# Kernel tuning notes

Measured on AMD Instinct MI355X. Metric: run time of the kernel, lower is better.

Reference implementation:

```python
import jax, jax.numpy as jnp
import numpy as np

T, N, D = 512, 1024, 256


def setup_inputs() -> dict:
    key = jax.random.key(0)
    k1, k2, k3, k4 = jax.random.split(key, 4)
    scale = 1.0 / np.sqrt(D)
    return {
        "H": jax.random.normal(k1, (T, N, D), dtype=jnp.float32),
        "fc_w": jax.random.normal(k2, (D, D), dtype=jnp.float32) * scale,
        "fc_b": jax.random.normal(k3, (D,), dtype=jnp.float32) * scale,
        "score_w": jax.random.normal(k4, (D,), dtype=jnp.float32) * scale,
    }


def _causal_attend(H, e):
    """C[t] = sum_{s<=t} softmax_{s<=t}(e[s]) * H[s], via online softmax scan.

    H: (T, N, D), e: (T, N) -> C: (T, N, D). O(T*N*D) time/memory.
    """
    n = H.shape[1]
    m0 = jnp.full((n,), -jnp.inf, dtype=H.dtype)   # running max of e
    s0 = jnp.zeros((n,), dtype=H.dtype)            # running softmax denom
    num0 = jnp.zeros((n, H.shape[2]), dtype=H.dtype)  # running weighted sum

    def step(carry, inp):
        m, s, num = carry
        e_t, h_t = inp  # (N,), (N, D)
        m_new = jnp.maximum(m, e_t)
        alpha = jnp.exp(m - m_new)          # rescale old accumulators
        p = jnp.exp(e_t - m_new)            # weight of current timestep
        s_new = s * alpha + p
        num_new = num * alpha[:, None] + p[:, None] * h_t
        c_t = num_new / s_new[:, None]
        return (m_new, s_new, num_new), c_t

    _, C = jax.lax.scan(step, (m0, s0, num0), (e, H))
    return C  # (T, N, D)


def reference(H, fc_w, fc_b, score_w):
    # Q = tanh(Linear(H)); e = score(Q)  -> (T, N)
    Q = jnp.tanh(jnp.einsum('tnd,ed->tne', H, fc_w) + fc_b)
    e = jnp.einsum('tne,e->tn', Q, score_w)
    return _causal_attend(H, e)
```

## Files before the change

kernel.cpp:

```cpp
#include <hip/hip_runtime.h>
#include <hip/hip_bf16.h>
#include <math.h>


#define T_DIM 512
#define N_DIM 1024
#define D_DIM 256

typedef short v8s __attribute__((ext_vector_type(8)));
typedef float v4f __attribute__((ext_vector_type(4)));

__device__ __forceinline__ unsigned pk_bf16(float a, float b) {
    unsigned ua = __builtin_bit_cast(unsigned, a);
    unsigned ub = __builtin_bit_cast(unsigned, b);
    ua = ua + 0x7fffu + ((ua >> 16) & 1u);
    ub = ub + 0x7fffu + ((ub >> 16) & 1u);
    return (ua >> 16) | (ub & 0xffff0000u);
}

__device__ __forceinline__ float fast_tanh(float x) {
    float e = __expf(2.0f * x);
    return 1.0f - 2.0f / (e + 1.0f);
}

__global__ __launch_bounds__(256, 2) void k_score(
    const float* __restrict__ H, const float* __restrict__ fc_w,
    const float* __restrict__ fc_b, const float* __restrict__ score_w,
    float* __restrict__ e_out)
{
    const int tid  = threadIdx.x;
    const int w    = tid >> 6;
    const int l    = tid & 63;
    const int l15  = l & 15;
    const int quad = l >> 4;

    v8s Bf[4][8];
#pragma unroll
    for (int jt = 0; jt < 4; ++jt) {
        const int j = w * 64 + jt * 16 + l15;
#pragma unroll
        for (int ks = 0; ks < 8; ++ks) {
            const int k = ks * 32 + quad * 8;
            const float4* p = (const float4*)(fc_w + j * D_DIM + k);
            float4 b0 = p[0], b1 = p[1];
            union { v8s v; unsigned u[4]; } bf;
            bf.u[0] = pk_bf16(b0.x, b0.y); bf.u[1] = pk_bf16(b0.z, b0.w);
            bf.u[2] = pk_bf16(b1.x, b1.y); bf.u[3] = pk_bf16(b1.z, b1.w);
            Bf[jt][ks] = bf.v;
        }
    }
    float fcb[4], scw[4];
#pragma unroll
    for (int jt = 0; jt < 4; ++jt) {
        const int j = w * 64 + jt * 16 + l15;
        fcb[jt] = fc_b[j];
        scw[jt] = score_w[j];
    }

    __shared__ float ebuf[4][16];

    const int n_tiles = (T_DIM * N_DIM) / 16;
    for (int mt = blockIdx.x; mt < n_tiles; mt += gridDim.x) {
        const float* hrow = H + (size_t)(mt * 16 + l15) * D_DIM + quad * 8;

        v4f acc[4];
        const v4f vz = {0.f, 0.f, 0.f, 0.f};
#pragma unroll
        for (int jt = 0; jt < 4; ++jt) acc[jt] = vz;

#pragma unroll
        for (int ks = 0; ks < 8; ++ks) {
            const float4* p = (const float4*)(hrow + ks * 32);
            float4 h0 = p[0], h1 = p[1];
            union { v8s v; unsigned u[4]; } af;
            af.u[0] = pk_bf16(h0.x, h0.y); af.u[1] = pk_bf16(h0.z, h0.w);
            af.u[2] = pk_bf16(h1.x, h1.y); af.u[3] = pk_bf16(h1.z, h1.w);
#pragma unroll
            for (int jt = 0; jt < 4; ++jt)
                acc[jt] = __builtin_amdgcn_mfma_f32_16x16x32_bf16(
                    af.v, Bf[jt][ks], acc[jt], 0, 0, 0);
        }

        float er[4];
#pragma unroll
        for (int r = 0; r < 4; ++r) {
            float s = 0.f;
#pragma unroll
            for (int jt = 0; jt < 4; ++jt) {
                float q = fast_tanh(acc[jt][r] + fcb[jt]);
                s += q * scw[jt];
            }
            er[r] = s;
        }
#pragma unroll
        for (int m = 1; m < 16; m <<= 1) {
#pragma unroll
            for (int r = 0; r < 4; ++r)
                er[r] += __shfl_xor(er[r], m, 64);
        }
        if (l15 == 0) {
#pragma unroll
            for (int r = 0; r < 4; ++r) ebuf[w][quad * 4 + r] = er[r];
        }
        __syncthreads();
        if (tid < 16) {
            float ev = ebuf[0][tid] + ebuf[1][tid] + ebuf[2][tid] + ebuf[3][tid];
            e_out[mt * 16 + tid] = ev;
        }
        __syncthreads();
    }
}

__global__ void k_coef(const float* __restrict__ e, float2* __restrict__ co)
{
    const int n = blockIdx.x * blockDim.x + threadIdx.x;
    float m = -INFINITY, s = 0.f;
    for (int t = 0; t < T_DIM; ++t) {
        float ev    = e[t * N_DIM + n];
        float mn    = fmaxf(m, ev);
        float alpha = __expf(m - mn);
        float p     = __expf(ev - mn);
        float sn    = s * alpha + p;
        float rs    = 1.0f / sn;
        co[t * N_DIM + n] = make_float2(alpha * s * rs, p * rs);
        m = mn; s = sn;
    }
}

__global__ __launch_bounds__(128) void k_apply(
    const float* __restrict__ H, const float2* __restrict__ co,
    float* __restrict__ C)
{
    const int n  = blockIdx.x;
    const int d2 = threadIdx.x;
    const float2* Hp = (const float2*)(H + (size_t)n * D_DIM) + d2;
    float2*       Cp = (float2*)(C + (size_t)n * D_DIM) + d2;
    const int stride2 = (N_DIM * D_DIM) / 2;

    float2 num = {0.f, 0.f};
    float2 h   = Hp[0];
    float2 ab  = co[n];
    for (int t = 0; t < T_DIM; ++t) {
        float2 hn = {0.f, 0.f};
        float2 abn = {0.f, 0.f};
        if (t + 1 < T_DIM) {
            hn  = Hp[(size_t)(t + 1) * stride2];
            abn = co[(t + 1) * N_DIM + n];
        }
        num.x = num.x * ab.x + ab.y * h.x;
        num.y = num.y * ab.x + ab.y * h.y;
        Cp[(size_t)t * stride2] = num;
        h = hn; ab = abn;
    }
}

extern "C" void kernel_launch(void* const* d_in, const int* in_sizes, int n_in,
                              void* d_out, int out_size, void* d_ws, size_t ws_size,
                              hipStream_t stream) {
    const float* H       = (const float*)d_in[0];
    const float* fc_w    = (const float*)d_in[1];
    const float* fc_b    = (const float*)d_in[2];
    const float* score_w = (const float*)d_in[3];
    float* C = (float*)d_out;

    float*  e  = (float*)d_ws;
    float2* co = (float2*)(e + T_DIM * N_DIM);

    k_score<<<dim3(512), dim3(256), 0, stream>>>(H, fc_w, fc_b, score_w, e);
    k_coef <<<dim3(4),   dim3(256), 0, stream>>>(e, co);
    k_apply<<<dim3(N_DIM), dim3(128), 0, stream>>>(H, co, C);
}
```

Measured before the change: 1.259 ms.

## Restructure score GEMM with LDS weights and fuse coefficient scan into apply

```diff
diff --git a/kernel.cpp b/kernel.cpp
--- a/kernel.cpp
+++ b/kernel.cpp
@@ -23,62 +23,76 @@
     return 1.0f - 2.0f / (e + 1.0f);
 }
 
-__global__ __launch_bounds__(256, 2) void k_score(
+#define SCORE_BLOCKS 256
+#define SCORE_WAVES  (SCORE_BLOCKS * 8)
+
+__global__ __launch_bounds__(512, 2) void k_score(
     const float* __restrict__ H, const float* __restrict__ fc_w,
     const float* __restrict__ fc_b, const float* __restrict__ score_w,
     float* __restrict__ e_out)
 {
+    __shared__ uint4 Bs[8192];
+
     const int tid  = threadIdx.x;
-    const int w    = tid >> 6;
     const int l    = tid & 63;
     const int l15  = l & 15;
     const int quad = l >> 4;
 
-    v8s Bf[4][8];
-#pragma unroll
-    for (int jt = 0; jt < 4; ++jt) {
-        const int j = w * 64 + jt * 16 + l15;
-#pragma unroll
-        for (int ks = 0; ks < 8; ++ks) {
-            const int k = ks * 32 + quad * 8;
-            const float4* p = (const float4*)(fc_w + j * D_DIM + k);
-            float4 b0 = p[0], b1 = p[1];
-            union { v8s v; unsigned u[4]; } bf;
-            bf.u[0] = pk_bf16(b0.x, b0.y); bf.u[1] = pk_bf16(b0.z, b0.w);
-            bf.u[2] = pk_bf16(b1.x, b1.y); bf.u[3] = pk_bf16(b1.z, b1.w);
-            Bf[jt][ks] = bf.v;
-        }
-    }
-    float fcb[4], scw[4];
-#pragma unroll
-    for (int jt = 0; jt < 4; ++jt) {
-        const int j = w * 64 + jt * 16 + l15;
-        fcb[jt] = fc_b[j];
-        scw[jt] = score_w[j];
-    }
-
-    __shared__ float ebuf[4][16];
-
+#pragma unroll
+    for (int r = 0; r < 16; ++r) {
+        int c  = r * 512 + tid;
+        int j  = c >> 5;
+        int q4 = c & 31;
+        const float4* p = (const float4*)(fc_w + j * D_DIM + q4 * 8);
+        float4 b0 = p[0], b1 = p[1];
+        uint4 u;
+        u.x = pk_bf16(b0.x, b0.y); u.y = pk_bf16(b0.z, b0.w);
+        u.z = pk_bf16(b1.x, b1.y); u.w = pk_bf16(b1.z, b1.w);
+        Bs[q4 * 256 + j] = u;
+    }
+
+    float fcb[16], scw[16];
+#pragma unroll
+    for (int jt = 0; jt < 16; ++jt) {
+        fcb[jt] = fc_b[jt * 16 + l15];
+        scw[jt] = score_w[jt * 16 + l15];
+    }
+
+    __syncthreads();
+
+    const v8s* Bv = (const v8s*)Bs;
+    const int cbase = quad * 256 + l15;
+
+    const int gw = blockIdx.x * 8 + (tid >> 6);
     const int n_tiles = (T_DIM * N_DIM) / 16;
-    for (int mt = blockIdx.x; mt < n_tiles; mt += gridDim.x) {
+
+    for (int mt = gw; mt < n_tiles; mt += SCORE_WAVES) {
         const float* hrow = H + (size_t)(mt * 16 + l15) * D_DIM + quad * 8;
 
-        v4f acc[4];
-        const v4f vz = {0.f, 0.f, 0.f, 0.f};
-#pragma unroll
-        for (int jt = 0; jt < 4; ++jt) acc[jt] = vz;
-
+        v8s af[8];
 #pragma unroll
         for (int ks = 0; ks < 8; ++ks) {
             const float4* p = (const float4*)(hrow + ks * 32);
-            float4 h0 = p[0], h1 = p[1];
-            union { v8s v; unsigned u[4]; } af;
-            af.u[0] = pk_bf16(h0.x, h0.y); af.u[1] = pk_bf16(h0.z, h0.w);
-            af.u[2] = pk_bf16(h1.x, h1.y); af.u[3] = pk_bf16(h1.z, h1.w);
-#pragma unroll
-            for (int jt = 0; jt < 4; ++jt)
+            float4 a0 = p[0], a1 = p[1];
+            union { v8s v; unsigned u[4]; } f;
+            f.u[0] = pk_bf16(a0.x, a0.y); f.u[1] = pk_bf16(a0.z, a0.w);
+            f.u[2] = pk_bf16(a1.x, a1.y); f.u[3] = pk_bf16(a1.z, a1.w);
+            af[ks] = f.v;
+        }
+
+        v4f acc[16];
+        const v4f vz = {0.f, 0.f, 0.f, 0.f};
+#pragma unroll
+        for (int jt = 0; jt < 16; ++jt) acc[jt] = vz;
+
+#pragma unroll
+        for (int ks = 0; ks < 8; ++ks) {
+#pragma unroll
+            for (int jt = 0; jt < 16; ++jt) {
+                v8s bf = Bv[ks * 1024 + jt * 16 + cbase];
                 acc[jt] = __builtin_amdgcn_mfma_f32_16x16x32_bf16(
-                    af.v, Bf[jt][ks], acc[jt], 0, 0, 0);
+                    af[ks], bf, acc[jt], 0, 0, 0);
+            }
         }
 
         float er[4];
@@ -86,71 +100,96 @@
         for (int r = 0; r < 4; ++r) {
             float s = 0.f;
 #pragma unroll
-            for (int jt = 0; jt < 4; ++jt) {
-                float q = fast_tanh(acc[jt][r] + fcb[jt]);
-                s += q * scw[jt];
-            }
+            for (int jt = 0; jt < 16; ++jt)
+                s += fast_tanh(acc[jt][r] + fcb[jt]) * scw[jt];
             er[r] = s;
         }
 #pragma unroll
-        for (int m = 1; m < 16; m <<= 1) {
+        for (int msk = 1; msk < 16; msk <<= 1) {
 #pragma unroll
             for (int r = 0; r < 4; ++r)
-                er[r] += __shfl_xor(er[r], m, 64);
+                er[r] += __shfl_xor(er[r], msk, 64);
         }
         if (l15 == 0) {
 #pragma unroll
-            for (int r = 0; r < 4; ++r) ebuf[w][quad * 4 + r] = er[r];
-        }
-        __syncthreads();
-        if (tid < 16) {
-            float ev = ebuf[0][tid] + ebuf[1][tid] + ebuf[2][tid] + ebuf[3][tid];
-            e_out[mt * 16 + tid] = ev;
-        }
-        __syncthreads();
-    }
-}
-
-__global__ void k_coef(const float* __restrict__ e, float2* __restrict__ co)
-{
-    const int n = blockIdx.x * blockDim.x + threadIdx.x;
-    float m = -INFINITY, s = 0.f;
-    for (int t = 0; t < T_DIM; ++t) {
-        float ev    = e[t * N_DIM + n];
-        float mn    = fmaxf(m, ev);
-        float alpha = __expf(m - mn);
-        float p     = __expf(ev - mn);
-        float sn    = s * alpha + p;
-        float rs    = 1.0f / sn;
-        co[t * N_DIM + n] = make_float2(alpha * s * rs, p * rs);
-        m = mn; s = sn;
-    }
-}
-
-__global__ __launch_bounds__(128) void k_apply(
-    const float* __restrict__ H, const float2* __restrict__ co,
+            for (int r = 0; r < 4; ++r)
+                e_out[mt * 16 + quad * 4 + r] = er[r];
+        }
+    }
+}
+
+__global__ __launch_bounds__(256) void k_apply(
+    const float* __restrict__ H, const float* __restrict__ e,
     float* __restrict__ C)
 {
-    const int n  = blockIdx.x;
-    const int d2 = threadIdx.x;
-    const float2* Hp = (const float2*)(H + (size_t)n * D_DIM) + d2;
-    float2*       Cp = (float2*)(C + (size_t)n * D_DIM) + d2;
-    const int stride2 = (N_DIM * D_DIM) / 2;
-
-    float2 num = {0.f, 0.f};
-    float2 h   = Hp[0];
-    float2 ab  = co[n];
+    __shared__ float2 coef[T_DIM];
+
+    const int n   = blockIdx.x;
+    const int tid = threadIdx.x;
+
+    if (tid < 64) {
+        float ev[8];
+#pragma unroll
+        for (int i = 0; i < 8; ++i)
+            ev[i] = e[(tid * 8 + i) * N_DIM + n];
+
+        float m = -INFINITY, s = 0.f;
+#pragma unroll
+        for (int i = 0; i < 8; ++i) {
+            float mn = fmaxf(m, ev[i]);
+            s = s * __expf(m - mn) + __expf(ev[i] - mn);
+            m = mn;
+        }
+#pragma unroll
+        for (int off = 1; off < 64; off <<= 1) {
+            float mo = __shfl_up(m, off, 64);
+            float so = __shfl_up(s, off, 64);
+            if (tid >= off) {
+                float mn = fmaxf(mo, m);
+                s = s * __expf(m - mn) + so * __expf(mo - mn);
+                m = mn;
+            }
+        }
+        float pm = __shfl_up(m, 1, 64);
+        float ps = __shfl_up(s, 1, 64);
+        if (tid == 0) { pm = -INFINITY; ps = 0.f; }
+
+        float mm = pm, ss = ps;
+#pragma unroll
+        for (int i = 0; i < 8; ++i) {
+            float et    = ev[i];
+            float mn    = fmaxf(mm, et);
+            float alpha = __expf(mm - mn);
+            float p     = __expf(et - mn);
+            float sn    = ss * alpha + p;
+            float rs    = 1.0f / sn;
+            coef[tid * 8 + i] = make_float2(alpha * ss * rs, p * rs);
+            mm = mn; ss = sn;
+        }
+    }
+    __syncthreads();
+
+    const size_t base = (size_t)n * D_DIM + tid;
+    const float* Hp = H + base;
+    float*       Cp = C + base;
+    const size_t st = (size_t)N_DIM * D_DIM;
+
+    float num = 0.f;
+    float  h0 = Hp[0],        h1 = Hp[st];
+    float  h2 = Hp[2 * st],   h3 = Hp[3 * st];
+    float2 a0 = coef[0], a1 = coef[1], a2 = coef[2], a3 = coef[3];
+
     for (int t = 0; t < T_DIM; ++t) {
-        float2 hn = {0.f, 0.f};
-        float2 abn = {0.f, 0.f};
-        if (t + 1 < T_DIM) {
-            hn  = Hp[(size_t)(t + 1) * stride2];
-            abn = co[(t + 1) * N_DIM + n];
-        }
-        num.x = num.x * ab.x + ab.y * h.x;
-        num.y = num.y * ab.x + ab.y * h.y;
-        Cp[(size_t)t * stride2] = num;
-        h = hn; ab = abn;
+        float  h4 = 0.f;
+        float2 a4 = make_float2(0.f, 0.f);
+        if (t + 4 < T_DIM) {
+            h4 = Hp[(size_t)(t + 4) * st];
+            a4 = coef[t + 4];
+        }
+        num = fmaf(num, a0.x, a0.y * h0);
+        Cp[(size_t)t * st] = num;
+        h0 = h1; h1 = h2; h2 = h3; h3 = h4;
+        a0 = a1; a1 = a2; a2 = a3; a3 = a4;
     }
 }
 
@@ -163,10 +202,8 @@
     const float* score_w = (const float*)d_in[3];
     float* C = (float*)d_out;
 
-    float*  e  = (float*)d_ws;
-    float2* co = (float2*)(e + T_DIM * N_DIM);
-
-    k_score<<<dim3(512), dim3(256), 0, stream>>>(H, fc_w, fc_b, score_w, e);
-    k_coef <<<dim3(4),   dim3(256), 0, stream>>>(e, co);
-    k_apply<<<dim3(N_DIM), dim3(128), 0, stream>>>(H, co, C);
-}
+    float* e = (float*)d_ws;
+
+    k_score<<<dim3(SCORE_BLOCKS), dim3(512), 0, stream>>>(H, fc_w, fc_b, score_w, e);
+    k_apply<<<dim3(N_DIM), dim3(256), 0, stream>>>(H, e, C);
+}
```

Result: slower. 1.763 ms (+40.0%).
